# Performance work log

Hardware: AMD Instinct MI355X
Metric: run time of the kernel (lower is better)

The kernel has to match this reference:

```python
import jax, jax.numpy as jnp
import numpy as np

N, D, H, E_DIM = 2048, 128, 8, 10
DH = D // H
EPS = 1e-5

def _ln(x, g, b):
    mu = jnp.mean(x, axis=-1, keepdims=True)
    var = jnp.mean((x - mu) ** 2, axis=-1, keepdims=True)
    return (x - mu) / jnp.sqrt(var + EPS) * g + b

def setup_inputs() -> dict:
    key = jax.random.key(0)
    ks = jax.random.split(key, 16)
    E = 65536
    inp = {
        "node_feat": jax.random.normal(ks[0], (N, D), jnp.float32),
        "edge_feat": jax.random.normal(ks[1], (E, E_DIM), jnp.float32),
        "src": jax.random.randint(ks[2], (E,), 0, N, jnp.int32).astype(jnp.int64),
        "dst": jax.random.randint(ks[3], (E,), 0, N, jnp.int32).astype(jnp.int64),
        "Wq": jax.random.normal(ks[4], (D, D), jnp.float32) * 0.02,
        "bq": jnp.zeros((D,), jnp.float32),
        "Wk": jax.random.normal(ks[5], (D, D), jnp.float32) * 0.02,
        "bk": jnp.zeros((D,), jnp.float32),
        "Wv": jax.random.normal(ks[6], (D, D), jnp.float32) * 0.02,
        "bv": jnp.zeros((D,), jnp.float32),
        "Wo": jax.random.normal(ks[7], (D, D), jnp.float32) * 0.02,
        "bo": jnp.zeros((D,), jnp.float32),
        "We": jax.random.normal(ks[8], (E_DIM, H), jnp.float32) * 0.02,
        "be": jnp.zeros((H,), jnp.float32),
        "g1": jnp.ones((D,), jnp.float32),
        "b1n": jnp.zeros((D,), jnp.float32),
        "g2": jnp.ones((D,), jnp.float32),
        "b2n": jnp.zeros((D,), jnp.float32),
        "W1": jax.random.normal(ks[9], (D, 4 * D), jnp.float32) * 0.02,
        "bf1": jnp.zeros((4 * D,), jnp.float32),
        "W2": jax.random.normal(ks[10], (4 * D, D), jnp.float32) * 0.02,
        "bf2": jnp.zeros((D,), jnp.float32),
    }
    return inp

def reference(node_feat, edge_feat, src, dst, Wq, bq, Wk, bk, Wv, bv, Wo, bo,
              We, be, g1, b1n, g2, b2n, W1, bf1, W2, bf2):
    n = node_feat.shape[0]
    Q = (node_feat @ Wq + bq).reshape(n, H, DH)
    K = (node_feat @ Wk + bk).reshape(n, H, DH)
    V = (node_feat @ Wv + bv).reshape(n, H, DH)
    scores = jnp.einsum('ihd,jhd->ijh', Q, K) / jnp.sqrt(jnp.float32(DH))
    # scatter edge bias into dense [N,N,H] (set semantics, like torch indexed assign)
    edge_bias = edge_feat @ We + be  # [E,H]
    bias = jnp.zeros((n, n, H), scores.dtype).at[src, dst].set(edge_bias)
    scores = scores + bias
    # symmetric adjacency mask with self-loops
    adj = jnp.zeros((n, n), scores.dtype)
    adj = adj.at[src, dst].set(1.0).at[dst, src].set(1.0)
    idx = jnp.arange(n)
    adj = adj.at[idx, idx].set(1.0)
    scores = jnp.where(adj[:, :, None] == 0, -jnp.inf, scores)
    attn = jax.nn.softmax(scores, axis=1)  # softmax over keys j (dim=1)
    out = jnp.einsum('ijh,jhd->ihd', attn, V).reshape(n, -1)
    out = out @ Wo + bo
    out = _ln(out + node_feat, g1, b1n)
    ffn = jax.nn.relu(out @ W1 + bf1) @ W2 + bf2
    out = _ln(out + ffn, g2, b2n)
    return out
```

## Files before the change

kernel.cpp:

```cpp
#include <hip/hip_runtime.h>
#include <hip/hip_bf16.h>

#define NN   2048
#define DDIM 128
#define HH   8
#define DHH  16
#define NEDGE 65536
#define FFN  512
#define EPSV 1e-5f
#define CAP  256

typedef const float* fp_c;

__device__ __forceinline__ bool idx64(const int* src) {
    return (src[1] | src[3] | src[5] | src[7] | src[9] | src[11]) == 0;
}

__global__ __launch_bounds__(512) void k_pq(float* Qf, float* Kf, float* Vf, fp_c x,
                                            fp_c Wq, fp_c bq, fp_c Wk, fp_c bk, fp_c Wv, fp_c bv,
                                            int* eid, unsigned* bm, float* eb,
                                            const int* src, const int* dst,
                                            fp_c edge_feat, fp_c We, fp_c be) {
    int b = blockIdx.x;
    int t = threadIdx.x;
    if (b < 512) {
        __shared__ float sx[4][DDIM];
        __shared__ float red[3][4][4][DDIM];
        int r0 = b * 4;
        int c = t & 127;
        int ks = t >> 7;
        sx[t >> 7][t & 127] = x[r0 * DDIM + t];
        __syncthreads();
        float aq[4] = {0, 0, 0, 0}, ak[4] = {0, 0, 0, 0}, av[4] = {0, 0, 0, 0};
        int kbeg = ks * 32;
#pragma unroll 8
        for (int k = kbeg; k < kbeg + 32; k++) {
            float wq = Wq[k * DDIM + c];
            float wk = Wk[k * DDIM + c];
            float wv = Wv[k * DDIM + c];
#pragma unroll
            for (int r = 0; r < 4; r++) {
                float xv = sx[r][k];
                aq[r] += xv * wq; ak[r] += xv * wk; av[r] += xv * wv;
            }
        }
#pragma unroll
        for (int r = 0; r < 4; r++) {
            red[0][ks][r][c] = aq[r];
            red[1][ks][r][c] = ak[r];
            red[2][ks][r][c] = av[r];
        }
        __syncthreads();
        int rr = t >> 7, cc = t & 127;
        float vq = 0, vk = 0, vv = 0;
#pragma unroll
        for (int s = 0; s < 4; s++) {
            vq += red[0][s][rr][cc];
            vk += red[1][s][rr][cc];
            vv += red[2][s][rr][cc];
        }
        Qf[(r0 + rr) * DDIM + cc] = (vq + bq[cc]) * 0.25f;
        Kf[(r0 + rr) * DDIM + cc] = vk + bk[cc];
        Vf[(r0 + rr) * DDIM + cc] = vv + bv[cc];
    } else {
        __shared__ float sWe[80];
        __shared__ float sbe[8];
        if (t < 80) sWe[t] = We[t];
        if (t < 8)  sbe[t] = be[t];
        __syncthreads();
        int u = (b - 512) * 512 + t;
        bool is64 = idx64(src);
        if (u < NN * 64 / 4) ((int4*)bm)[u] = make_int4(0, 0, 0, 0);
        if (u < NN) eid[u * NN + u] = -2;
        if (u < NEDGE) {
            int s = is64 ? src[2 * u] : src[u];
            int d = is64 ? dst[2 * u] : dst[u];
            eid[s * NN + d] = -2;
            eid[d * NN + s] = -2;
            float ef[10];
#pragma unroll
            for (int k = 0; k < 10; k++) ef[k] = edge_feat[u * 10 + k];
#pragma unroll
            for (int h = 0; h < 8; h++) {
                float a = sbe[h];
#pragma unroll
                for (int k = 0; k < 10; k++) a += ef[k] * sWe[k * 8 + h];
                eb[u * 8 + h] = a;
            }
        }
    }
}

__global__ __launch_bounds__(512) void k_scatter(int* eid, unsigned* bm, const int* src, const int* dst) {
    int t = blockIdx.x * blockDim.x + threadIdx.x;
    bool is64 = idx64(src);
    if (t < NEDGE) {
        int s = is64 ? src[2 * t] : src[t];
        int d = is64 ? dst[2 * t] : dst[t];
        atomicMax(&eid[s * NN + d], t);
        atomicOr(&bm[s * 64 + (d >> 5)], 1u << (d & 31));
        atomicOr(&bm[d * 64 + (s >> 5)], 1u << (s & 31));
    } else if (t < NEDGE + NN) {
        int i = t - NEDGE;
        atomicOr(&bm[i * 64 + (i >> 5)], 1u << (i & 31));
    }
}

__global__ __launch_bounds__(256) void k_attn(float* attn_out, const float* Qf, const float* Kf,
                                              const float* Vf, const int* eid, const float* eb,
                                              const unsigned* bm) {
    __shared__ float qrow[DDIM];
    __shared__ int   lj[CAP + 8];
    __shared__ int   lev[CAP + 8];
    __shared__ float sc[CAP + 8][HH];
    __shared__ float hinv[HH];
    __shared__ float redpv[2][DDIM];
    __shared__ int   scnt;
    int i = blockIdx.x;
    int t = threadIdx.x;
    if (t < 128) qrow[t] = Qf[i * DDIM + t];

    if (t < 64) {
        unsigned word = bm[i * 64 + t];
        int pc = __popc(word);
        int x = pc;
#pragma unroll
        for (int off = 1; off < 64; off <<= 1) {
            int y = __shfl_up(x, off);
            if (t >= off) x += y;
        }
        int cnt = __shfl(x, 63);
        if (cnt > CAP - 8) cnt = CAP - 8;
        int idx = x - pc;
        unsigned w = word;
        while (w && idx < CAP) {
            int bpos = __ffs(w) - 1;
            lj[idx++] = (t << 5) + bpos;
            w &= w - 1;
        }
        if (t < 8) lj[cnt + t] = 0;
        if (t == 0) scnt = cnt;
    }
    __syncthreads();
    int cnt = scnt;
    int cnt8 = (cnt + 7) & ~7;
    if (t < cnt8) lev[t] = (t < cnt) ? eid[(long)i * NN + lj[t]] : -2;
    __syncthreads();

    int h = t & 7;
    int nsl = t >> 3;
    const float4* q4 = (const float4*)(qrow + h * DHH);
    float4 q0 = q4[0], q1 = q4[1], q2 = q4[2], q3 = q4[3];
    for (int n = nsl; n < cnt8; n += 32) {
        int j = lj[n];
        const float4* k4 = (const float4*)(Kf + j * DDIM + h * DHH);
        float4 k0 = k4[0], k1 = k4[1], k2 = k4[2], k3 = k4[3];
        float s = q0.x * k0.x + q0.y * k0.y + q0.z * k0.z + q0.w * k0.w
                + q1.x * k1.x + q1.y * k1.y + q1.z * k1.z + q1.w * k1.w
                + q2.x * k2.x + q2.y * k2.y + q2.z * k2.z + q2.w * k2.w
                + q3.x * k3.x + q3.y * k3.y + q3.z * k3.z + q3.w * k3.w;
        int ev = lev[n];
        if (ev >= 0) s += eb[ev * 8 + h];
        sc[n][h] = s;
    }
    __syncthreads();

    {
        int hh = t >> 5;
        int sub = t & 31;
        float m = -1e30f;
        for (int n = sub; n < cnt; n += 32) m = fmaxf(m, sc[n][hh]);
#pragma unroll
        for (int off = 1; off < 32; off <<= 1) m = fmaxf(m, __shfl_xor(m, off));
        float ssum = 0.f;
        for (int n = sub; n < cnt; n += 32) {
            float e = __expf(sc[n][hh] - m);
            sc[n][hh] = e;
            ssum += e;
        }
#pragma unroll
        for (int off = 1; off < 32; off <<= 1) ssum += __shfl_xor(ssum, off);
        if (sub == 0) hinv[hh] = 1.0f / ssum;
    }
    if (t < 64) {
        int p = cnt + (t >> 3);
        if (p < cnt8) sc[p][t & 7] = 0.f;
    }
    __syncthreads();

    {
        int g = t >> 7, c = t & 127, h2 = c >> 4;
        float a = 0.f;
#pragma unroll 4
        for (int n = g; n < cnt8; n += 2)
            a += sc[n][h2] * Vf[lj[n] * DDIM + c];
        redpv[g][c] = a;
    }
    __syncthreads();
    if (t < 128)
        attn_out[i * DDIM + t] = (redpv[0][t] + redpv[1][t]) * hinv[t >> 4];
}

__global__ __launch_bounds__(512) void k_tail(float* out, const float* ain,
                                              fp_c Wo, fp_c bo, fp_c node, fp_c g1, fp_c b1,
                                              fp_c W1, fp_c bf1, fp_c W2, fp_c bf2,
                                              fp_c g2, fp_c b2) {
    __shared__ float sa[4][DDIM];
    __shared__ float red[4][4][DDIM];
    __shared__ float x1ld[4][DDIM];
    __shared__ float sh[4][FFN];
    __shared__ float2 sc2[8];
    int t = threadIdx.x;
    int r0 = blockIdx.x * 4;
    int c = t & 127;
    int ks = t >> 7;
    int rr = t >> 7, cc = t & 127;
    sa[t >> 7][t & 127] = ain[r0 * DDIM + t];
    __syncthreads();

    {
        float acc[4] = {0, 0, 0, 0};
        int kbeg = ks * 32;
#pragma unroll 8
        for (int k = kbeg; k < kbeg + 32; k++) {
            float w = Wo[k * DDIM + c];
#pragma unroll
            for (int r = 0; r < 4; r++) acc[r] += sa[r][k] * w;
        }
#pragma unroll
        for (int r = 0; r < 4; r++) red[ks][r][c] = acc[r];
        __syncthreads();
        float val = red[0][rr][cc] + red[1][rr][cc] + red[2][rr][cc] + red[3][rr][cc];
        val += bo[cc] + node[(r0 + rr) * DDIM + cc];
        float vs = val, vq = val * val;
#pragma unroll
        for (int off = 32; off >= 1; off >>= 1) {
            vs += __shfl_down(vs, off);
            vq += __shfl_down(vq, off);
        }
        if ((t & 63) == 0) sc2[t >> 6] = make_float2(vs, vq);
        __syncthreads();
        float sum = sc2[2 * rr].x + sc2[2 * rr + 1].x;
        float sq  = sc2[2 * rr].y + sc2[2 * rr + 1].y;
        float mu = sum * (1.0f / DDIM);
        float var = sq * (1.0f / DDIM) - mu * mu;
        x1ld[rr][cc] = (val - mu) * rsqrtf(var + EPSV) * g1[cc] + b1[cc];
    }
    __syncthreads();

    {
        float acc[4] = {0, 0, 0, 0};
#pragma unroll 8
        for (int k = 0; k < DDIM; k++) {
            float w = W1[k * FFN + t];
#pragma unroll
            for (int r = 0; r < 4; r++) acc[r] += x1ld[r][k] * w;
        }
        float bb = bf1[t];
#pragma unroll
        for (int r = 0; r < 4; r++) sh[r][t] = fmaxf(acc[r] + bb, 0.f);
    }
    __syncthreads();

    {
        float acc[4] = {0, 0, 0, 0};
        int kbeg = ks * 128;
#pragma unroll 8
        for (int k = kbeg; k < kbeg + 128; k++) {
            float w = W2[k * DDIM + c];
#pragma unroll
            for (int r = 0; r < 4; r++) acc[r] += sh[r][k] * w;
        }
#pragma unroll
        for (int r = 0; r < 4; r++) red[ks][r][c] = acc[r];
        __syncthreads();
        float val = red[0][rr][cc] + red[1][rr][cc] + red[2][rr][cc] + red[3][rr][cc];
        val += bf2[cc] + x1ld[rr][cc];
        float vs = val, vq = val * val;
#pragma unroll
        for (int off = 32; off >= 1; off >>= 1) {
            vs += __shfl_down(vs, off);
            vq += __shfl_down(vq, off);
        }
        if ((t & 63) == 0) sc2[t >> 6] = make_float2(vs, vq);
        __syncthreads();
        float sum = sc2[2 * rr].x + sc2[2 * rr + 1].x;
        float sq  = sc2[2 * rr].y + sc2[2 * rr + 1].y;
        float mu = sum * (1.0f / DDIM);
        float var = sq * (1.0f / DDIM) - mu * mu;
        out[(r0 + rr) * DDIM + cc] = (val - mu) * rsqrtf(var + EPSV) * g2[cc] + b2[cc];
    }
}

extern "C" void kernel_launch(void* const* d_in, const int* in_sizes, int n_in,
                              void* d_out, int out_size, void* d_ws, size_t ws_size,
                              hipStream_t stream) {
    fp_c node = (fp_c)d_in[0];
    fp_c edge_feat = (fp_c)d_in[1];
    const int* src = (const int*)d_in[2];
    const int* dst = (const int*)d_in[3];
    fp_c Wq = (fp_c)d_in[4];  fp_c bq = (fp_c)d_in[5];
    fp_c Wk = (fp_c)d_in[6];  fp_c bk = (fp_c)d_in[7];
    fp_c Wv = (fp_c)d_in[8];  fp_c bv = (fp_c)d_in[9];
    fp_c Wo = (fp_c)d_in[10]; fp_c bo = (fp_c)d_in[11];
    fp_c We = (fp_c)d_in[12]; fp_c be = (fp_c)d_in[13];
    fp_c g1 = (fp_c)d_in[14]; fp_c b1n = (fp_c)d_in[15];
    fp_c g2 = (fp_c)d_in[16]; fp_c b2n = (fp_c)d_in[17];
    fp_c W1 = (fp_c)d_in[18]; fp_c bf1 = (fp_c)d_in[19];
    fp_c W2 = (fp_c)d_in[20]; fp_c bf2 = (fp_c)d_in[21];

    char* ws = (char*)d_ws;
    int* eid      = (int*)ws;      ws += (size_t)NN * NN * 4;
    unsigned* bm  = (unsigned*)ws; ws += (size_t)NN * 64 * 4;
    float* eb     = (float*)ws;    ws += (size_t)NEDGE * 8 * 4;
    float* Qf     = (float*)ws;    ws += (size_t)NN * DDIM * 4;
    float* Kf     = (float*)ws;    ws += (size_t)NN * DDIM * 4;
    float* Vf     = (float*)ws;    ws += (size_t)NN * DDIM * 4;
    float* attn_o = (float*)ws;    ws += (size_t)NN * DDIM * 4;

    k_pq<<<768, 512, 0, stream>>>(Qf, Kf, Vf, node, Wq, bq, Wk, bk, Wv, bv,
                                  eid, bm, eb, src, dst, edge_feat, We, be);
    k_scatter<<<(NEDGE + NN + 511) / 512, 512, 0, stream>>>(eid, bm, src, dst);
    k_attn<<<NN, 256, 0, stream>>>(attn_o, Qf, Kf, Vf, eid, eb, bm);
    k_tail<<<NN / 4, 512, 0, stream>>>((float*)d_out, attn_o, Wo, bo, node, g1, b1n,
                                       W1, bf1, W2, bf2, g2, b2n);
}
```

Measured before the change: 68.38 us.

## Fuse sparse attention with output projection, LayerNorm and FFN tail kernel

Merges the per-node attention kernel into the tail kernel. Each 512-thread block now handles four nodes: it computes attention for two nodes at a time in two passes, keeps the results in shared memory, then runs the Wo/LN/FFN/LN tail. This drops one kernel launch and the global round trip of the attention output. In exchange the grid falls from 2048 blocks to 512, which reduces parallelism for the irregular gather-heavy attention phase and adds barriers.

```diff
diff --git a/kernel.cpp b/kernel.cpp
--- a/kernel.cpp
+++ b/kernel.cpp
@@ -3,7 +3,7 @@
 
 #define NN   2048
 #define DDIM 128
-#define HH   8
+#define HH    8
 #define DHH  16
 #define NEDGE 65536
 #define FFN  512
@@ -29,7 +29,7 @@
         int r0 = b * 4;
         int c = t & 127;
         int ks = t >> 7;
-        sx[t >> 7][t & 127] = x[r0 * DDIM + t];
+        sx[ks][c] = x[r0 * DDIM + t];
         __syncthreads();
         float aq[4] = {0, 0, 0, 0}, ak[4] = {0, 0, 0, 0}, av[4] = {0, 0, 0, 0};
         int kbeg = ks * 32;
@@ -71,12 +71,12 @@
         int u = (b - 512) * 512 + t;
         bool is64 = idx64(src);
         if (u < NN * 64 / 4) ((int4*)bm)[u] = make_int4(0, 0, 0, 0);
-        if (u < NN) eid[u * NN + u] = -2;
+        if (u < NN) eid[(long)u * NN + u] = -2;
         if (u < NEDGE) {
             int s = is64 ? src[2 * u] : src[u];
             int d = is64 ? dst[2 * u] : dst[u];
-            eid[s * NN + d] = -2;
-            eid[d * NN + s] = -2;
+            eid[(long)s * NN + d] = -2;
+            eid[(long)d * NN + s] = -2;
             float ef[10];
 #pragma unroll
             for (int k = 0; k < 10; k++) ef[k] = edge_feat[u * 10 + k];
@@ -91,13 +91,14 @@
     }
 }
 
-__global__ __launch_bounds__(512) void k_scatter(int* eid, unsigned* bm, const int* src, const int* dst) {
+__global__ __launch_bounds__(512) void k_scatter(int* eid, unsigned* bm,
+                                                 const int* src, const int* dst) {
     int t = blockIdx.x * blockDim.x + threadIdx.x;
     bool is64 = idx64(src);
     if (t < NEDGE) {
         int s = is64 ? src[2 * t] : src[t];
         int d = is64 ? dst[2 * t] : dst[t];
-        atomicMax(&eid[s * NN + d], t);
+        atomicMax(&eid[(long)s * NN + d], t);
         atomicOr(&bm[s * 64 + (d >> 5)], 1u << (d & 31));
         atomicOr(&bm[d * 64 + (s >> 5)], 1u << (s & 31));
     } else if (t < NEDGE + NN) {
@@ -106,118 +107,115 @@
     }
 }
 
-__global__ __launch_bounds__(256) void k_attn(float* attn_out, const float* Qf, const float* Kf,
-                                              const float* Vf, const int* eid, const float* eb,
-                                              const unsigned* bm) {
-    __shared__ float qrow[DDIM];
-    __shared__ int   lj[CAP + 8];
-    __shared__ int   lev[CAP + 8];
-    __shared__ float sc[CAP + 8][HH];
-    __shared__ float hinv[HH];
-    __shared__ float redpv[2][DDIM];
-    __shared__ int   scnt;
-    int i = blockIdx.x;
-    int t = threadIdx.x;
-    if (t < 128) qrow[t] = Qf[i * DDIM + t];
-
-    if (t < 64) {
-        unsigned word = bm[i * 64 + t];
-        int pc = __popc(word);
-        int x = pc;
-#pragma unroll
-        for (int off = 1; off < 64; off <<= 1) {
-            int y = __shfl_up(x, off);
-            if (t >= off) x += y;
-        }
-        int cnt = __shfl(x, 63);
-        if (cnt > CAP - 8) cnt = CAP - 8;
-        int idx = x - pc;
-        unsigned w = word;
-        while (w && idx < CAP) {
-            int bpos = __ffs(w) - 1;
-            lj[idx++] = (t << 5) + bpos;
-            w &= w - 1;
-        }
-        if (t < 8) lj[cnt + t] = 0;
-        if (t == 0) scnt = cnt;
+__global__ __launch_bounds__(512) void k_at(float* out, const float* Qf, const float* Kf,
+                                            const float* Vf, const int* eid, const float* eb,
+                                            const unsigned* bm,
+                                            fp_c Wo, fp_c bo, fp_c node, fp_c g1, fp_c b1,
+                                            fp_c W1, fp_c bf1, fp_c W2, fp_c bf2,
+                                            fp_c g2, fp_c b2) {
+    union Smem {
+        struct { float qrow[2][DDIM]; int lj[2][CAP + 8]; int lev[2][CAP + 8];
+                 float sc[2][CAP + 8][HH]; float hinv[2][HH];
+                 float redpv[2][2][DDIM]; int scnt[2]; } a;
+        struct { float red[4][4][DDIM]; float x1[4][DDIM]; float sh[4][FFN];
+                 float2 sc2[8]; } tl;
+    };
+    __shared__ Smem S;
+    __shared__ float ao[4][DDIM];
+    int b = blockIdx.x, t = threadIdx.x;
+
+    int gi = t >> 8;
+    int t2 = t & 255;
+#pragma unroll 1
+    for (int p = 0; p < 2; p++) {
+        __syncthreads();
+        int il = p * 2 + gi;
+        int i = b * 4 + il;
+        if (t2 < 128) S.a.qrow[gi][t2] = Qf[i * DDIM + t2];
+        if (t2 < 64) {
+            unsigned word = bm[i * 64 + t2];
+            int pc = __popc(word);
+            int x = pc;
+#pragma unroll
+            for (int off = 1; off < 64; off <<= 1) {
+                int y = __shfl_up(x, off);
+                if (t2 >= off) x += y;
+            }
+            int cnt = __shfl(x, 63);
+            if (cnt > CAP - 8) cnt = CAP - 8;
+            int idx = x - pc;
+            unsigned w = word;
+            while (w && idx < CAP) {
+                int bp = __ffs(w) - 1;
+                S.a.lj[gi][idx++] = (t2 << 5) + bp;
+                w &= w - 1;
+            }
+            if (t2 < 8) S.a.lj[gi][cnt + t2] = 0;
+            if (t2 == 0) S.a.scnt[gi] = cnt;
+        }
+        __syncthreads();
+        int cnt = S.a.scnt[gi];
+        int cnt8 = (cnt + 7) & ~7;
+        if (t2 < cnt8)
+            S.a.lev[gi][t2] = (t2 < cnt) ? eid[(long)i * NN + S.a.lj[gi][t2]] : -1;
+        __syncthreads();
+        {
+            int h = t2 & 7, nsl = t2 >> 3;
+            const float4* q4 = (const float4*)(&S.a.qrow[gi][h * DHH]);
+            float4 q0 = q4[0], q1 = q4[1], q2 = q4[2], q3 = q4[3];
+            for (int n = nsl; n < cnt8; n += 32) {
+                int j = S.a.lj[gi][n];
+                const float4* k4 = (const float4*)(Kf + j * DDIM + h * DHH);
+                float4 k0 = k4[0], k1 = k4[1], k2 = k4[2], k3 = k4[3];
+                float s = q0.x * k0.x + q0.y * k0.y + q0.z * k0.z + q0.w * k0.w
+                        + q1.x * k1.x + q1.y * k1.y + q1.z * k1.z + q1.w * k1.w
+                        + q2.x * k2.x + q2.y * k2.y + q2.z * k2.z + q2.w * k2.w
+                        + q3.x * k3.x + q3.y * k3.y + q3.z * k3.z + q3.w * k3.w;
+                int ev = S.a.lev[gi][n];
+                if (ev >= 0) s += eb[ev * 8 + h];
+                S.a.sc[gi][n][h] = s;
+            }
+        }
+        __syncthreads();
+        {
+            int hh = t2 >> 5, sub = t2 & 31;
+            float m = -1e30f;
+            for (int n = sub; n < cnt; n += 32) m = fmaxf(m, S.a.sc[gi][n][hh]);
+#pragma unroll
+            for (int off = 1; off < 32; off <<= 1) m = fmaxf(m, __shfl_xor(m, off));
+            float ssum = 0.f;
+            for (int n = sub; n < cnt; n += 32) {
+                float e = __expf(S.a.sc[gi][n][hh] - m);
+                S.a.sc[gi][n][hh] = e;
+                ssum += e;
+            }
+#pragma unroll
+            for (int off = 1; off < 32; off <<= 1) ssum += __shfl_xor(ssum, off);
+            if (sub == 0) S.a.hinv[gi][hh] = 1.0f / ssum;
+        }
+        if (t2 < 64) {
+            int pp = cnt + (t2 >> 3);
+            if (pp < cnt8) S.a.sc[gi][pp][t2 & 7] = 0.f;
+        }
+        __syncthreads();
+        {
+            int gg = t2 >> 7, c = t2 & 127, h2 = c >> 4;
+            float a = 0.f;
+#pragma unroll 4
+            for (int n = gg; n < cnt8; n += 2)
+                a += S.a.sc[gi][n][h2] * Vf[S.a.lj[gi][n] * DDIM + c];
+            S.a.redpv[gi][gg][c] = a;
+        }
+        __syncthreads();
+        if (t2 < 128)
+            ao[il][t2] = (S.a.redpv[gi][0][t2] + S.a.redpv[gi][1][t2]) * S.a.hinv[gi][t2 >> 4];
     }
     __syncthreads();
-    int cnt = scnt;
-    int cnt8 = (cnt + 7) & ~7;
-    if (t < cnt8) lev[t] = (t < cnt) ? eid[(long)i * NN + lj[t]] : -2;
-    __syncthreads();
-
-    int h = t & 7;
-    int nsl = t >> 3;
-    const float4* q4 = (const float4*)(qrow + h * DHH);
-    float4 q0 = q4[0], q1 = q4[1], q2 = q4[2], q3 = q4[3];
-    for (int n = nsl; n < cnt8; n += 32) {
-        int j = lj[n];
-        const float4* k4 = (const float4*)(Kf + j * DDIM + h * DHH);
-        float4 k0 = k4[0], k1 = k4[1], k2 = k4[2], k3 = k4[3];
-        float s = q0.x * k0.x + q0.y * k0.y + q0.z * k0.z + q0.w * k0.w
-                + q1.x * k1.x + q1.y * k1.y + q1.z * k1.z + q1.w * k1.w
-                + q2.x * k2.x + q2.y * k2.y + q2.z * k2.z + q2.w * k2.w
-                + q3.x * k3.x + q3.y * k3.y + q3.z * k3.z + q3.w * k3.w;
-        int ev = lev[n];
-        if (ev >= 0) s += eb[ev * 8 + h];
-        sc[n][h] = s;
-    }
-    __syncthreads();
-
-    {
-        int hh = t >> 5;
-        int sub = t & 31;
-        float m = -1e30f;
-        for (int n = sub; n < cnt; n += 32) m = fmaxf(m, sc[n][hh]);
-#pragma unroll
-        for (int off = 1; off < 32; off <<= 1) m = fmaxf(m, __shfl_xor(m, off));
-        float ssum = 0.f;
-        for (int n = sub; n < cnt; n += 32) {
-            float e = __expf(sc[n][hh] - m);
-            sc[n][hh] = e;
-            ssum += e;
-        }
-#pragma unroll
-        for (int off = 1; off < 32; off <<= 1) ssum += __shfl_xor(ssum, off);
-        if (sub == 0) hinv[hh] = 1.0f / ssum;
-    }
-    if (t < 64) {
-        int p = cnt + (t >> 3);
-        if (p < cnt8) sc[p][t & 7] = 0.f;
-    }
-    __syncthreads();
-
-    {
-        int g = t >> 7, c = t & 127, h2 = c >> 4;
-        float a = 0.f;
-#pragma unroll 4
-        for (int n = g; n < cnt8; n += 2)
-            a += sc[n][h2] * Vf[lj[n] * DDIM + c];
-        redpv[g][c] = a;
-    }
-    __syncthreads();
-    if (t < 128)
-        attn_out[i * DDIM + t] = (redpv[0][t] + redpv[1][t]) * hinv[t >> 4];
-}
-
-__global__ __launch_bounds__(512) void k_tail(float* out, const float* ain,
-                                              fp_c Wo, fp_c bo, fp_c node, fp_c g1, fp_c b1,
-                                              fp_c W1, fp_c bf1, fp_c W2, fp_c bf2,
-                                              fp_c g2, fp_c b2) {
-    __shared__ float sa[4][DDIM];
-    __shared__ float red[4][4][DDIM];
-    __shared__ float x1ld[4][DDIM];
-    __shared__ float sh[4][FFN];
-    __shared__ float2 sc2[8];
-    int t = threadIdx.x;
-    int r0 = blockIdx.x * 4;
+
+    int r0 = b * 4;
     int c = t & 127;
     int ks = t >> 7;
     int rr = t >> 7, cc = t & 127;
-    sa[t >> 7][t & 127] = ain[r0 * DDIM + t];
-    __syncthreads();
-
     {
         float acc[4] = {0, 0, 0, 0};
         int kbeg = ks * 32;
@@ -225,12 +223,13 @@
         for (int k = kbeg; k < kbeg + 32; k++) {
             float w = Wo[k * DDIM + c];
 #pragma unroll
-            for (int r = 0; r < 4; r++) acc[r] += sa[r][k] * w;
-        }
-#pragma unroll
-        for (int r = 0; r < 4; r++) red[ks][r][c] = acc[r];
-        __syncthreads();
-        float val = red[0][rr][cc] + red[1][rr][cc] + red[2][rr][cc] + red[3][rr][cc];
+            for (int r = 0; r < 4; r++) acc[r] += ao[r][k] * w;
+        }
+#pragma unroll
+        for (int r = 0; r < 4; r++) S.tl.red[ks][r][c] = acc[r];
+        __syncthreads();
+        float val = S.tl.red[0][rr][cc] + S.tl.red[1][rr][cc]
+                  + S.tl.red[2][rr][cc] + S.tl.red[3][rr][cc];
         val += bo[cc] + node[(r0 + rr) * DDIM + cc];
         float vs = val, vq = val * val;
 #pragma unroll
@@ -238,30 +237,28 @@
             vs += __shfl_down(vs, off);
             vq += __shfl_down(vq, off);
         }
-        if ((t & 63) == 0) sc2[t >> 6] = make_float2(vs, vq);
-        __syncthreads();
-        float sum = sc2[2 * rr].x + sc2[2 * rr + 1].x;
-        float sq  = sc2[2 * rr].y + sc2[2 * rr + 1].y;
+        if ((t & 63) == 0) S.tl.sc2[t >> 6] = make_float2(vs, vq);
+        __syncthreads();
+        float sum = S.tl.sc2[2 * rr].x + S.tl.sc2[2 * rr + 1].x;
+        float sq  = S.tl.sc2[2 * rr].y + S.tl.sc2[2 * rr + 1].y;
         float mu = sum * (1.0f / DDIM);
         float var = sq * (1.0f / DDIM) - mu * mu;
-        x1ld[rr][cc] = (val - mu) * rsqrtf(var + EPSV) * g1[cc] + b1[cc];
+        S.tl.x1[rr][cc] = (val - mu) * rsqrtf(var + EPSV) * g1[cc] + b1[cc];
     }
     __syncthreads();
-
     {
         float acc[4] = {0, 0, 0, 0};
 #pragma unroll 8
         for (int k = 0; k < DDIM; k++) {
             float w = W1[k * FFN + t];
 #pragma unroll
-            for (int r = 0; r < 4; r++) acc[r] += x1ld[r][k] * w;
+            for (int r = 0; r < 4; r++) acc[r] += S.tl.x1[r][k] * w;
         }
         float bb = bf1[t];
 #pragma unroll
-        for (int r = 0; r < 4; r++) sh[r][t] = fmaxf(acc[r] + bb, 0.f);
+        for (int r = 0; r < 4; r++) S.tl.sh[r][t] = fmaxf(acc[r] + bb, 0.f);
     }
     __syncthreads();
-
     {
         float acc[4] = {0, 0, 0, 0};
         int kbeg = ks * 128;
@@ -269,23 +266,24 @@
         for (int k = kbeg; k < kbeg + 128; k++) {
             float w = W2[k * DDIM + c];
 #pragma unroll
-            for (int r = 0; r < 4; r++) acc[r] += sh[r][k] * w;
-        }
-#pragma unroll
-        for (int r = 0; r < 4; r++) red[ks][r][c] = acc[r];
-        __syncthreads();
-        float val = red[0][rr][cc] + red[1][rr][cc] + red[2][rr][cc] + red[3][rr][cc];
-        val += bf2[cc] + x1ld[rr][cc];
+            for (int r = 0; r < 4; r++) acc[r] += S.tl.sh[r][k] * w;
+        }
+#pragma unroll
+        for (int r = 0; r < 4; r++) S.tl.red[ks][r][c] = acc[r];
+        __syncthreads();
+        float val = S.tl.red[0][rr][cc] + S.tl.red[1][rr][cc]
+                  + S.tl.red[2][rr][cc] + S.tl.red[3][rr][cc];
+        val += bf2[cc] + S.tl.x1[rr][cc];
         float vs = val, vq = val * val;
 #pragma unroll
         for (int off = 32; off >= 1; off >>= 1) {
             vs += __shfl_down(vs, off);
             vq += __shfl_down(vq, off);
         }
-        if ((t & 63) == 0) sc2[t >> 6] = make_float2(vs, vq);
-        __syncthreads();
-        float sum = sc2[2 * rr].x + sc2[2 * rr + 1].x;
-        float sq  = sc2[2 * rr].y + sc2[2 * rr + 1].y;
+        if ((t & 63) == 0) S.tl.sc2[t >> 6] = make_float2(vs, vq);
+        __syncthreads();
+        float sum = S.tl.sc2[2 * rr].x + S.tl.sc2[2 * rr + 1].x;
+        float sq  = S.tl.sc2[2 * rr].y + S.tl.sc2[2 * rr + 1].y;
         float mu = sum * (1.0f / DDIM);
         float var = sq * (1.0f / DDIM) - mu * mu;
         out[(r0 + rr) * DDIM + cc] = (val - mu) * rsqrtf(var + EPSV) * g2[cc] + b2[cc];
@@ -310,18 +308,16 @@
     fp_c W2 = (fp_c)d_in[20]; fp_c bf2 = (fp_c)d_in[21];
 
     char* ws = (char*)d_ws;
-    int* eid      = (int*)ws;      ws += (size_t)NN * NN * 4;
-    unsigned* bm  = (unsigned*)ws; ws += (size_t)NN * 64 * 4;
-    float* eb     = (float*)ws;    ws += (size_t)NEDGE * 8 * 4;
-    float* Qf     = (float*)ws;    ws += (size_t)NN * DDIM * 4;
-    float* Kf     = (float*)ws;    ws += (size_t)NN * DDIM * 4;
-    float* Vf     = (float*)ws;    ws += (size_t)NN * DDIM * 4;
-    float* attn_o = (float*)ws;    ws += (size_t)NN * DDIM * 4;
+    int* eid     = (int*)ws;      ws += (size_t)NN * NN * 4;
+    unsigned* bm = (unsigned*)ws; ws += (size_t)NN * 64 * 4;
+    float* eb    = (float*)ws;    ws += (size_t)NEDGE * 8 * 4;
+    float* Qf    = (float*)ws;    ws += (size_t)NN * DDIM * 4;
+    float* Kf    = (float*)ws;    ws += (size_t)NN * DDIM * 4;
+    float* Vf    = (float*)ws;    ws += (size_t)NN * DDIM * 4;
 
     k_pq<<<768, 512, 0, stream>>>(Qf, Kf, Vf, node, Wq, bq, Wk, bk, Wv, bv,
                                   eid, bm, eb, src, dst, edge_feat, We, be);
     k_scatter<<<(NEDGE + NN + 511) / 512, 512, 0, stream>>>(eid, bm, src, dst);
-    k_attn<<<NN, 256, 0, stream>>>(attn_o, Qf, Kf, Vf, eid, eb, bm);
-    k_tail<<<NN / 4, 512, 0, stream>>>((float*)d_out, attn_o, Wo, bo, node, g1, b1n,
-                                       W1, bf1, W2, bf2, g2, b2n);
-}
+    k_at<<<NN / 4, 512, 0, stream>>>((float*)d_out, Qf, Kf, Vf, eid, eb, bm,
+                                     Wo, bo, node, g1, b1n, W1, bf1, W2, bf2, g2, b2n);
+}
```

New measurement: 71.42 us. +4.5%, slower.
